# Kernel tuning notes

Hardware: AMD Instinct MI355X
Metric: run time of the kernel (lower is better)

Reference implementation:

```python
import jax, jax.numpy as jnp
import numpy as np

B, S, D = 4, 4096, 768
E, SLOTS = 16, 1  # n_experts, slots_per_expert
H = 4 * D


def setup_inputs() -> dict:
    key = jax.random.key(0)
    k = jax.random.split(key, 6)
    scale1 = 1.0 / np.sqrt(D)
    scale2 = 1.0 / np.sqrt(H)
    return {
        "x": jax.random.normal(k[0], (B, S, D), dtype=jnp.float32),
        "phi": jax.random.normal(k[1], (D, E * SLOTS), dtype=jnp.float32),
        "W1": jax.random.normal(k[2], (E, D, H), dtype=jnp.float32) * scale1,
        "b1": jnp.zeros((E, H), dtype=jnp.float32),
        "W2": jax.random.normal(k[3], (E, H, D), dtype=jnp.float32) * scale2,
        "b2": jnp.zeros((E, D), dtype=jnp.float32),
    }


def reference(x, phi, W1, b1, W2, b2):
    # logits: [B, S, E*SLOTS]
    logits = jnp.einsum("bsd,dn->bsn", x, phi)
    dispatch_weights = jax.nn.softmax(logits, axis=-1)  # over slots
    combine_weights = jax.nn.softmax(logits, axis=1)    # over sequence
    # xs: [B, E*SLOTS, D] = dispatch^T @ x
    xs = jnp.einsum("bsn,bsd->bnd", dispatch_weights, x)
    xs = xs.reshape(B, E, SLOTS, D)
    # per-expert FFN, batched over experts: GELU (exact, as torch nn.GELU default)
    h = jnp.einsum("bepd,edh->beph", xs, W1) + b1[None, :, None, :]
    h = jax.nn.gelu(h, approximate=False)
    ys = jnp.einsum("beph,ehd->bepd", h, W2) + b2[None, :, None, :]
    ys = ys.reshape(B, E * SLOTS, D)
    # combine: [B, S, D]
    y = jnp.einsum("bsn,bnd->bsd", combine_weights, ys)
    return y
```

## Files before the change

kernel.cpp:

```cpp
#include <hip/hip_runtime.h>
#include <math.h>

constexpr int B = 4, S = 4096, D = 768, E = 16, N = 16, H = 3072;
constexpr int HL = 96;
constexpr int NHC = H / HL;
constexpr int LBLK = 32;
constexpr int LPB = S / LBLK;

constexpr size_t OFF_LOG  = 0;
constexpr size_t OFF_PCM  = OFF_LOG + (size_t)B * S * N;
constexpr size_t OFF_PCS  = OFF_PCM + (size_t)B * LPB * N;
constexpr size_t OFF_CMAX = OFF_PCS + (size_t)B * LPB * N;
constexpr size_t OFF_CSUM = OFF_CMAX + (size_t)B * N;
constexpr size_t OFF_XSP  = OFF_CSUM + (size_t)B * N;
constexpr size_t OFF_XS   = OFF_XSP + (size_t)B * LPB * N * D;
constexpr size_t OFF_YSP  = OFF_XS + (size_t)B * N * D;
constexpr size_t OFF_YS   = OFF_YSP + (size_t)NHC * B * E * D;

__device__ __forceinline__ void fma4(float4& a, float s, const float4& w) {
    a.x = fmaf(s, w.x, a.x);
    a.y = fmaf(s, w.y, a.y);
    a.z = fmaf(s, w.z, a.z);
    a.w = fmaf(s, w.w, a.w);
}

__global__ __launch_bounds__(256) void k_lx(const float* __restrict__ x,
                                            const float* __restrict__ phi,
                                            float* __restrict__ logits,
                                            float* __restrict__ xsp,
                                            float* __restrict__ pcm,
                                            float* __restrict__ pcs) {
    __shared__ float ph[16][D];
    __shared__ float xr[LBLK][D + 4];
    __shared__ float dwl[LBLK][16];
    __shared__ float rm[16][16], rs[16][16];
    const int t = threadIdx.x;
    const int blk = blockIdx.x;
    const int b = blk / LPB;
    const int s0 = (blk % LPB) * LBLK;

#pragma unroll
    for (int i = 0; i < 12; ++i) {
        const int idx = i * 1024 + t * 4;
        const float4 v = *reinterpret_cast<const float4*>(phi + idx);
        const int d0 = idx >> 4;
        const int n0 = idx & 15;
        ph[n0 + 0][d0] = v.x;
        ph[n0 + 1][d0] = v.y;
        ph[n0 + 2][d0] = v.z;
        ph[n0 + 3][d0] = v.w;
    }
    const float* xsrc = x + ((size_t)b * S + s0) * D;
#pragma unroll
    for (int i = 0; i < 24; ++i) {
        const int idx = i * 256 + t;
        const int r = idx / 192, c = idx % 192;
        *reinterpret_cast<float4*>(&xr[r][c * 4]) =
            *reinterpret_cast<const float4*>(xsrc + (size_t)idx * 4);
    }
    __syncthreads();

    const int gid = t >> 4;
    const int ln = t & 15;
    const int r0 = gid * 2, r1 = r0 + 1;

    float4 a0[12], a1[12];
#pragma unroll
    for (int j = 0; j < 12; ++j) {
        a0[j] = *reinterpret_cast<const float4*>(&xr[r0][j * 64 + ln * 4]);
        a1[j] = *reinterpret_cast<const float4*>(&xr[r1][j * 64 + ln * 4]);
    }
    float p0[16], p1[16];
#pragma unroll
    for (int n = 0; n < 16; ++n) {
        float q0 = 0.f, q1 = 0.f;
#pragma unroll
        for (int j = 0; j < 12; ++j) {
            const float4 pv = *reinterpret_cast<const float4*>(&ph[n][j * 64 + ln * 4]);
            q0 = fmaf(a0[j].x, pv.x, q0); q1 = fmaf(a1[j].x, pv.x, q1);
            q0 = fmaf(a0[j].y, pv.y, q0); q1 = fmaf(a1[j].y, pv.y, q1);
            q0 = fmaf(a0[j].z, pv.z, q0); q1 = fmaf(a1[j].z, pv.z, q1);
            q0 = fmaf(a0[j].w, pv.w, q0); q1 = fmaf(a1[j].w, pv.w, q1);
        }
        p0[n] = q0; p1[n] = q1;
    }
#pragma unroll
    for (int m = 1; m < 16; m <<= 1) {
#pragma unroll
        for (int n = 0; n < 16; ++n) {
            p0[n] += __shfl_xor(p0[n], m, 64);
            p1[n] += __shfl_xor(p1[n], m, 64);
        }
    }
    float m0 = -1e30f, m1 = -1e30f;
#pragma unroll
    for (int n = 0; n < 16; ++n) { m0 = fmaxf(m0, p0[n]); m1 = fmaxf(m1, p1[n]); }
    float su0 = 0.f, su1 = 0.f;
#pragma unroll
    for (int n = 0; n < 16; ++n) { su0 += __expf(p0[n] - m0); su1 += __expf(p1[n] - m1); }
    const size_t o0 = ((size_t)b * S + s0 + r0) * N + ln;
    logits[o0] = p0[ln];
    logits[o0 + N] = p1[ln];
    dwl[r0][ln] = __expf(p0[ln] - m0) / su0;
    dwl[r1][ln] = __expf(p1[ln] - m1) / su1;

    const float mm = fmaxf(p0[ln], p1[ln]);
    rm[gid][ln] = mm;
    rs[gid][ln] = __expf(p0[ln] - mm) + __expf(p1[ln] - mm);
    __syncthreads();

    if (t < 16) {
        float M = -1e30f;
#pragma unroll
        for (int g = 0; g < 16; ++g) M = fmaxf(M, rm[g][t]);
        float SS = 0.f;
#pragma unroll
        for (int g = 0; g < 16; ++g) SS += rs[g][t] * __expf(rm[g][t] - M);
        pcm[blk * 16 + t] = M;
        pcs[blk * 16 + t] = SS;
    }

    if (t < 192) {
        const int d4 = t * 4;
        float4 a[16];
#pragma unroll
        for (int n = 0; n < 16; ++n) a[n] = float4{0.f, 0.f, 0.f, 0.f};
#pragma unroll 4
        for (int s = 0; s < LBLK; ++s) {
            const float4 xv = *reinterpret_cast<const float4*>(&xr[s][d4]);
#pragma unroll
            for (int n = 0; n < 16; ++n) {
                const float w = dwl[s][n];
                a[n].x = fmaf(w, xv.x, a[n].x);
                a[n].y = fmaf(w, xv.y, a[n].y);
                a[n].z = fmaf(w, xv.z, a[n].z);
                a[n].w = fmaf(w, xv.w, a[n].w);
            }
        }
        float* o = xsp + (size_t)blk * N * D + d4;
#pragma unroll
        for (int n = 0; n < 16; ++n)
            *reinterpret_cast<float4*>(o + (size_t)n * D) = a[n];
    }
}

__global__ __launch_bounds__(256) void k_xsred_cmerge(const float* __restrict__ xsp,
                                                      float* __restrict__ xs,
                                                      const float* __restrict__ pcm,
                                                      const float* __restrict__ pcs,
                                                      float* __restrict__ cmax,
                                                      float* __restrict__ csum) {
    const int t = threadIdx.x;
    if (blockIdx.x < 192) {
        const int i = blockIdx.x * 256 + t;
        const int b = i / (N * D);
        const int rem = i % (N * D);
        const float* p = xsp + (size_t)b * LPB * N * D + rem;
        float sum = 0.f;
#pragma unroll 4
        for (int c = 0; c < LPB; ++c) sum += p[(size_t)c * N * D];
        xs[i] = sum;
    } else if (t < 64) {
        const int b = t >> 4, n = t & 15;
        float M = -1e30f;
#pragma unroll 8
        for (int c = 0; c < LPB; ++c) M = fmaxf(M, pcm[((size_t)b * LPB + c) * 16 + n]);
        float SS = 0.f;
#pragma unroll 8
        for (int c = 0; c < LPB; ++c)
            SS += pcs[((size_t)b * LPB + c) * 16 + n] * __expf(pcm[((size_t)b * LPB + c) * 16 + n] - M);
        cmax[b * 16 + n] = M;
        csum[b * 16 + n] = SS;
    }
}

__global__ __launch_bounds__(384) void k_ffn(const float* __restrict__ xs,
                                             const float* __restrict__ W1,
                                             const float* __restrict__ b1,
                                             const float* __restrict__ W2,
                                             float* __restrict__ ysp) {
    __shared__ __align__(16) float xs_lds[D][4];
    __shared__ __align__(16) float red[32][HL][4];
    __shared__ __align__(16) float h_lds[HL][4];

    const int t = threadIdx.x;
    const int e = blockIdx.x / NHC;
    const int hc = blockIdx.x % NHC;
    const int h0 = hc * HL;

    for (int idx = t; idx < D; idx += 384) {
#pragma unroll
        for (int b = 0; b < 4; ++b)
            xs_lds[idx][b] = xs[((size_t)b * N + e) * D + idx];
    }
    __syncthreads();

    {
        const int q = t / 12;
        const int cg = t % 12;
        const int c4a = cg * 4, c4b = 48 + cg * 4;
        float4 aA[4], aB[4];
#pragma unroll
        for (int b = 0; b < 4; ++b) { aA[b] = float4{0,0,0,0}; aB[b] = float4{0,0,0,0}; }
        const float* w1p = W1 + ((size_t)e * D + (size_t)q * 24) * H + h0;
#pragma unroll 8
        for (int dd = 0; dd < 24; ++dd) {
            const float* row = w1p + (size_t)dd * H;
            const float4 wa = *reinterpret_cast<const float4*>(row + c4a);
            const float4 wb = *reinterpret_cast<const float4*>(row + c4b);
            const float* xv = &xs_lds[q * 24 + dd][0];
            const float x0 = xv[0], x1 = xv[1], x2 = xv[2], x3 = xv[3];
            fma4(aA[0], x0, wa); fma4(aB[0], x0, wb);
            fma4(aA[1], x1, wa); fma4(aB[1], x1, wb);
            fma4(aA[2], x2, wa); fma4(aB[2], x2, wb);
            fma4(aA[3], x3, wa); fma4(aB[3], x3, wb);
        }
        *reinterpret_cast<float4*>(&red[q][c4a + 0][0]) = float4{aA[0].x, aA[1].x, aA[2].x, aA[3].x};
        *reinterpret_cast<float4*>(&red[q][c4a + 1][0]) = float4{aA[0].y, aA[1].y, aA[2].y, aA[3].y};
        *reinterpret_cast<float4*>(&red[q][c4a + 2][0]) = float4{aA[0].z, aA[1].z, aA[2].z, aA[3].z};
        *reinterpret_cast<float4*>(&red[q][c4a + 3][0]) = float4{aA[0].w, aA[1].w, aA[2].w, aA[3].w};
        *reinterpret_cast<float4*>(&red[q][c4b + 0][0]) = float4{aB[0].x, aB[1].x, aB[2].x, aB[3].x};
        *reinterpret_cast<float4*>(&red[q][c4b + 1][0]) = float4{aB[0].y, aB[1].y, aB[2].y, aB[3].y};
        *reinterpret_cast<float4*>(&red[q][c4b + 2][0]) = float4{aB[0].z, aB[1].z, aB[2].z, aB[3].z};
        *reinterpret_cast<float4*>(&red[q][c4b + 3][0]) = float4{aB[0].w, aB[1].w, aB[2].w, aB[3].w};
    }
    __syncthreads();

    {
        const int col = t >> 2, b = t & 3;
        float s = 0.f;
#pragma unroll
        for (int q = 0; q < 32; ++q) s += red[q][col][b];
        s += b1[(size_t)e * H + h0 + col];
        s = 0.5f * s * (1.0f + erff(s * 0.70710678118654752f));
        h_lds[col][b] = s;
    }
    __syncthreads();

    const int kq = t / 96;
    const int dg = t % 96;
    const int d4a = dg * 4, d4b = 384 + dg * 4;
    float4 yA[4], yB[4];
#pragma unroll
    for (int b = 0; b < 4; ++b) { yA[b] = float4{0,0,0,0}; yB[b] = float4{0,0,0,0}; }
    {
        const float* w2p = W2 + ((size_t)e * H + h0 + (size_t)kq * 24) * D;
#pragma unroll 8
        for (int kk = 0; kk < 24; ++kk) {
            const float* row = w2p + (size_t)kk * D;
            const float4 wa = *reinterpret_cast<const float4*>(row + d4a);
            const float4 wb = *reinterpret_cast<const float4*>(row + d4b);
            const float* hv = &h_lds[kq * 24 + kk][0];
            fma4(yA[0], hv[0], wa); fma4(yB[0], hv[0], wb);
            fma4(yA[1], hv[1], wa); fma4(yB[1], hv[1], wb);
            fma4(yA[2], hv[2], wa); fma4(yB[2], hv[2], wb);
            fma4(yA[3], hv[3], wa); fma4(yB[3], hv[3], wb);
        }
    }
    float4* pb = reinterpret_cast<float4*>(&red[0][0][0]);
    __syncthreads();
    if (kq > 0) {
        const int base = ((kq - 1) * 96 + dg) * 8;
#pragma unroll
        for (int b = 0; b < 4; ++b) {
            pb[base + b * 2 + 0] = yA[b];
            pb[base + b * 2 + 1] = yB[b];
        }
    }
    __syncthreads();
    if (kq == 0) {
#pragma unroll
        for (int b = 0; b < 4; ++b) {
            float4 rA = yA[b], rB = yB[b];
#pragma unroll
            for (int p = 0; p < 3; ++p) {
                const int base = (p * 96 + dg) * 8 + b * 2;
                const float4 uA = pb[base + 0], uB = pb[base + 1];
                rA.x += uA.x; rA.y += uA.y; rA.z += uA.z; rA.w += uA.w;
                rB.x += uB.x; rB.y += uB.y; rB.z += uB.z; rB.w += uB.w;
            }
            float* o = ysp + (((size_t)hc * B + b) * E + e) * D;
            *reinterpret_cast<float4*>(o + d4a) = rA;
            *reinterpret_cast<float4*>(o + d4b) = rB;
        }
    }
}

__global__ __launch_bounds__(256) void k_ysred(const float* __restrict__ ysp,
                                               const float* __restrict__ b2,
                                               float* __restrict__ ys) {
    const int i4 = blockIdx.x * 256 + threadIdx.x;
    const int rem4 = i4 % (E * D / 4);
    float4 v = *reinterpret_cast<const float4*>(b2 + (size_t)rem4 * 4);
#pragma unroll 8
    for (int p = 0; p < NHC; ++p) {
        const float4 u = *reinterpret_cast<const float4*>(ysp + (size_t)p * B * E * D + (size_t)i4 * 4);
        v.x += u.x; v.y += u.y; v.z += u.z; v.w += u.w;
    }
    *reinterpret_cast<float4*>(ys + (size_t)i4 * 4) = v;
}

__global__ __launch_bounds__(192) void k_combine(const float* __restrict__ logits,
                                                 const float* __restrict__ cmax,
                                                 const float* __restrict__ csum,
                                                 const float* __restrict__ ys,
                                                 float* __restrict__ y) {
    const int blk = blockIdx.x;
    const int b = blk / (S / 8);
    const int s0 = (blk % (S / 8)) * 8;
    const int t = threadIdx.x;
    const int d4 = t * 4;

    float4 ysr[16];
    float cm[16], ci[16];
#pragma unroll
    for (int n = 0; n < 16; ++n) {
        ysr[n] = *reinterpret_cast<const float4*>(ys + ((size_t)b * N + n) * D + d4);
        cm[n] = cmax[b * N + n];
        ci[n] = 1.0f / csum[b * N + n];
    }
#pragma unroll
    for (int r = 0; r < 8; ++r) {
        const int s = s0 + r;
        const float* lrow = logits + ((size_t)b * S + s) * N;
        float4 acc{0, 0, 0, 0};
#pragma unroll
        for (int n = 0; n < 16; ++n) {
            const float cw = __expf(lrow[n] - cm[n]) * ci[n];
            acc.x = fmaf(cw, ysr[n].x, acc.x);
            acc.y = fmaf(cw, ysr[n].y, acc.y);
            acc.z = fmaf(cw, ysr[n].z, acc.z);
            acc.w = fmaf(cw, ysr[n].w, acc.w);
        }
        *reinterpret_cast<float4*>(y + ((size_t)b * S + s) * D + d4) = acc;
    }
}

extern "C" void kernel_launch(void* const* d_in, const int* in_sizes, int n_in,
                              void* d_out, int out_size, void* d_ws, size_t ws_size,
                              hipStream_t stream) {
    const float* x   = (const float*)d_in[0];
    const float* phi = (const float*)d_in[1];
    const float* W1  = (const float*)d_in[2];
    const float* b1  = (const float*)d_in[3];
    const float* W2  = (const float*)d_in[4];
    const float* b2  = (const float*)d_in[5];
    float* y = (float*)d_out;
    float* ws = (float*)d_ws;

    float* logits = ws + OFF_LOG;
    float* pcm    = ws + OFF_PCM;
    float* pcs    = ws + OFF_PCS;
    float* cmax   = ws + OFF_CMAX;
    float* csum   = ws + OFF_CSUM;
    float* xsp    = ws + OFF_XSP;
    float* xs     = ws + OFF_XS;
    float* ysp    = ws + OFF_YSP;
    float* ys     = ws + OFF_YS;

    k_lx<<<B * LPB, 256, 0, stream>>>(x, phi, logits, xsp, pcm, pcs);
    k_xsred_cmerge<<<193, 256, 0, stream>>>(xsp, xs, pcm, pcs, cmax, csum);
    k_ffn<<<E * NHC, 384, 0, stream>>>(xs, W1, b1, W2, ysp);
    k_ysred<<<48, 256, 0, stream>>>(ysp, b2, ys);
    k_combine<<<B * (S / 8), 192, 0, stream>>>(logits, cmax, csum, ys, y);
}
```

Baseline: 154.1 us.

## Double-buffer nontemporal weight loads in expert FFN with deeper per-thread K chunks

```diff
diff --git a/kernel.cpp b/kernel.cpp
--- a/kernel.cpp
+++ b/kernel.cpp
@@ -17,7 +17,12 @@
 constexpr size_t OFF_YSP  = OFF_XS + (size_t)B * N * D;
 constexpr size_t OFF_YS   = OFF_YSP + (size_t)NHC * B * E * D;
 
-__device__ __forceinline__ void fma4(float4& a, float s, const float4& w) {
+typedef float vf4 __attribute__((ext_vector_type(4)));
+
+__device__ __forceinline__ vf4 ntl(const float* p) {
+    return __builtin_nontemporal_load(reinterpret_cast<const vf4*>(p));
+}
+__device__ __forceinline__ void fma4(float4& a, float s, const vf4& w) {
     a.x = fmaf(s, w.x, a.x);
     a.y = fmaf(s, w.y, a.y);
     a.z = fmaf(s, w.z, a.z);
@@ -180,7 +185,7 @@
                                              const float* __restrict__ W2,
                                              float* __restrict__ ysp) {
     __shared__ __align__(16) float xs_lds[D][4];
-    __shared__ __align__(16) float red[32][HL][4];
+    __shared__ __align__(16) float red_lds[16][HL][4];
     __shared__ __align__(16) float h_lds[HL][4];
 
     const int t = threadIdx.x;
@@ -196,33 +201,42 @@
     __syncthreads();
 
     {
-        const int q = t / 12;
-        const int cg = t % 12;
-        const int c4a = cg * 4, c4b = 48 + cg * 4;
-        float4 aA[4], aB[4];
-#pragma unroll
-        for (int b = 0; b < 4; ++b) { aA[b] = float4{0,0,0,0}; aB[b] = float4{0,0,0,0}; }
-        const float* w1p = W1 + ((size_t)e * D + (size_t)q * 24) * H + h0;
-#pragma unroll 8
-        for (int dd = 0; dd < 24; ++dd) {
-            const float* row = w1p + (size_t)dd * H;
-            const float4 wa = *reinterpret_cast<const float4*>(row + c4a);
-            const float4 wb = *reinterpret_cast<const float4*>(row + c4b);
-            const float* xv = &xs_lds[q * 24 + dd][0];
-            const float x0 = xv[0], x1 = xv[1], x2 = xv[2], x3 = xv[3];
-            fma4(aA[0], x0, wa); fma4(aB[0], x0, wb);
-            fma4(aA[1], x1, wa); fma4(aB[1], x1, wb);
-            fma4(aA[2], x2, wa); fma4(aB[2], x2, wb);
-            fma4(aA[3], x3, wa); fma4(aB[3], x3, wb);
-        }
-        *reinterpret_cast<float4*>(&red[q][c4a + 0][0]) = float4{aA[0].x, aA[1].x, aA[2].x, aA[3].x};
-        *reinterpret_cast<float4*>(&red[q][c4a + 1][0]) = float4{aA[0].y, aA[1].y, aA[2].y, aA[3].y};
-        *reinterpret_cast<float4*>(&red[q][c4a + 2][0]) = float4{aA[0].z, aA[1].z, aA[2].z, aA[3].z};
-        *reinterpret_cast<float4*>(&red[q][c4a + 3][0]) = float4{aA[0].w, aA[1].w, aA[2].w, aA[3].w};
-        *reinterpret_cast<float4*>(&red[q][c4b + 0][0]) = float4{aB[0].x, aB[1].x, aB[2].x, aB[3].x};
-        *reinterpret_cast<float4*>(&red[q][c4b + 1][0]) = float4{aB[0].y, aB[1].y, aB[2].y, aB[3].y};
-        *reinterpret_cast<float4*>(&red[q][c4b + 2][0]) = float4{aB[0].z, aB[1].z, aB[2].z, aB[3].z};
-        *reinterpret_cast<float4*>(&red[q][c4b + 3][0]) = float4{aB[0].w, aB[1].w, aB[2].w, aB[3].w};
+        const int c4 = (t % 24) * 4;
+        const int q = t / 24;
+        const float* w1p = W1 + ((size_t)e * D + (size_t)q * 48) * H + h0 + c4;
+        float4 a0{0,0,0,0}, a1{0,0,0,0}, a2{0,0,0,0}, a3{0,0,0,0};
+        vf4 bufA[8], bufB[8];
+#pragma unroll
+        for (int i = 0; i < 8; ++i) bufA[i] = ntl(w1p + (size_t)i * H);
+
+#define P1_STAGE(CUR, NXT, CH, PRE)                                          \
+        {                                                                    \
+            if (PRE) {                                                       \
+                _Pragma("unroll")                                            \
+                for (int i = 0; i < 8; ++i)                                  \
+                    NXT[i] = ntl(w1p + (size_t)((CH + 1) * 8 + i) * H);      \
+            }                                                                \
+            _Pragma("unroll")                                                \
+            for (int i = 0; i < 8; ++i) {                                    \
+                const float* xv = &xs_lds[q * 48 + CH * 8 + i][0];           \
+                fma4(a0, xv[0], CUR[i]);                                     \
+                fma4(a1, xv[1], CUR[i]);                                     \
+                fma4(a2, xv[2], CUR[i]);                                     \
+                fma4(a3, xv[3], CUR[i]);                                     \
+            }                                                                \
+        }
+        P1_STAGE(bufA, bufB, 0, 1)
+        P1_STAGE(bufB, bufA, 1, 1)
+        P1_STAGE(bufA, bufB, 2, 1)
+        P1_STAGE(bufB, bufA, 3, 1)
+        P1_STAGE(bufA, bufB, 4, 1)
+        P1_STAGE(bufB, bufA, 5, 0)
+#undef P1_STAGE
+
+        *reinterpret_cast<float4*>(&red_lds[q][c4 + 0][0]) = float4{a0.x, a1.x, a2.x, a3.x};
+        *reinterpret_cast<float4*>(&red_lds[q][c4 + 1][0]) = float4{a0.y, a1.y, a2.y, a3.y};
+        *reinterpret_cast<float4*>(&red_lds[q][c4 + 2][0]) = float4{a0.z, a1.z, a2.z, a3.z};
+        *reinterpret_cast<float4*>(&red_lds[q][c4 + 3][0]) = float4{a0.w, a1.w, a2.w, a3.w};
     }
     __syncthreads();
 
@@ -230,59 +244,73 @@
         const int col = t >> 2, b = t & 3;
         float s = 0.f;
 #pragma unroll
-        for (int q = 0; q < 32; ++q) s += red[q][col][b];
+        for (int q = 0; q < 16; ++q) s += red_lds[q][col][b];
         s += b1[(size_t)e * H + h0 + col];
         s = 0.5f * s * (1.0f + erff(s * 0.70710678118654752f));
         h_lds[col][b] = s;
     }
     __syncthreads();
 
-    const int kq = t / 96;
-    const int dg = t % 96;
-    const int d4a = dg * 4, d4b = 384 + dg * 4;
-    float4 yA[4], yB[4];
-#pragma unroll
-    for (int b = 0; b < 4; ++b) { yA[b] = float4{0,0,0,0}; yB[b] = float4{0,0,0,0}; }
+    const int dgrp = t % 192;
+    const int kq = t / 192;
+    float4 y0{0,0,0,0}, y1{0,0,0,0}, y2{0,0,0,0}, y3{0,0,0,0};
     {
-        const float* w2p = W2 + ((size_t)e * H + h0 + (size_t)kq * 24) * D;
-#pragma unroll 8
-        for (int kk = 0; kk < 24; ++kk) {
-            const float* row = w2p + (size_t)kk * D;
-            const float4 wa = *reinterpret_cast<const float4*>(row + d4a);
-            const float4 wb = *reinterpret_cast<const float4*>(row + d4b);
-            const float* hv = &h_lds[kq * 24 + kk][0];
-            fma4(yA[0], hv[0], wa); fma4(yB[0], hv[0], wb);
-            fma4(yA[1], hv[1], wa); fma4(yB[1], hv[1], wb);
-            fma4(yA[2], hv[2], wa); fma4(yB[2], hv[2], wb);
-            fma4(yA[3], hv[3], wa); fma4(yB[3], hv[3], wb);
-        }
-    }
-    float4* pb = reinterpret_cast<float4*>(&red[0][0][0]);
-    __syncthreads();
-    if (kq > 0) {
-        const int base = ((kq - 1) * 96 + dg) * 8;
-#pragma unroll
-        for (int b = 0; b < 4; ++b) {
-            pb[base + b * 2 + 0] = yA[b];
-            pb[base + b * 2 + 1] = yB[b];
-        }
+        const float* w2p = W2 + ((size_t)e * H + h0 + (size_t)kq * 48) * D + dgrp * 4;
+        vf4 bufA[8], bufB[8];
+#pragma unroll
+        for (int i = 0; i < 8; ++i) bufA[i] = ntl(w2p + (size_t)i * D);
+
+#define P2_STAGE(CUR, NXT, CH, PRE)                                          \
+        {                                                                    \
+            if (PRE) {                                                       \
+                _Pragma("unroll")                                            \
+                for (int i = 0; i < 8; ++i)                                  \
+                    NXT[i] = ntl(w2p + (size_t)((CH + 1) * 8 + i) * D);      \
+            }                                                                \
+            _Pragma("unroll")                                                \
+            for (int i = 0; i < 8; ++i) {                                    \
+                const float* hv = &h_lds[kq * 48 + CH * 8 + i][0];           \
+                fma4(y0, hv[0], CUR[i]);                                     \
+                fma4(y1, hv[1], CUR[i]);                                     \
+                fma4(y2, hv[2], CUR[i]);                                     \
+                fma4(y3, hv[3], CUR[i]);                                     \
+            }                                                                \
+        }
+        P2_STAGE(bufA, bufB, 0, 1)
+        P2_STAGE(bufB, bufA, 1, 1)
+        P2_STAGE(bufA, bufB, 2, 1)
+        P2_STAGE(bufB, bufA, 3, 1)
+        P2_STAGE(bufA, bufB, 4, 1)
+        P2_STAGE(bufB, bufA, 5, 0)
+#undef P2_STAGE
+    }
+
+    float4* pbuf = reinterpret_cast<float4*>(&xs_lds[0][0]);
+    __syncthreads();
+    if (kq == 1) {
+        pbuf[dgrp * 4 + 0] = y0;
+        pbuf[dgrp * 4 + 1] = y1;
+        pbuf[dgrp * 4 + 2] = y2;
+        pbuf[dgrp * 4 + 3] = y3;
     }
     __syncthreads();
     if (kq == 0) {
-#pragma unroll
-        for (int b = 0; b < 4; ++b) {
-            float4 rA = yA[b], rB = yB[b];
-#pragma unroll
-            for (int p = 0; p < 3; ++p) {
-                const int base = (p * 96 + dg) * 8 + b * 2;
-                const float4 uA = pb[base + 0], uB = pb[base + 1];
-                rA.x += uA.x; rA.y += uA.y; rA.z += uA.z; rA.w += uA.w;
-                rB.x += uB.x; rB.y += uB.y; rB.z += uB.z; rB.w += uB.w;
-            }
-            float* o = ysp + (((size_t)hc * B + b) * E + e) * D;
-            *reinterpret_cast<float4*>(o + d4a) = rA;
-            *reinterpret_cast<float4*>(o + d4b) = rB;
-        }
+        float4 r0 = pbuf[dgrp * 4 + 0];
+        float4 r1 = pbuf[dgrp * 4 + 1];
+        float4 r2 = pbuf[dgrp * 4 + 2];
+        float4 r3 = pbuf[dgrp * 4 + 3];
+        r0.x += y0.x; r0.y += y0.y; r0.z += y0.z; r0.w += y0.w;
+        r1.x += y1.x; r1.y += y1.y; r1.z += y1.z; r1.w += y1.w;
+        r2.x += y2.x; r2.y += y2.y; r2.z += y2.z; r2.w += y2.w;
+        r3.x += y3.x; r3.y += y3.y; r3.z += y3.z; r3.w += y3.w;
+        float* o0 = ysp + (((size_t)hc * B + 0) * E + e) * D + dgrp * 4;
+        float* o1 = ysp + (((size_t)hc * B + 1) * E + e) * D + dgrp * 4;
+        float* o2 = ysp + (((size_t)hc * B + 2) * E + e) * D + dgrp * 4;
+        float* o3 = ysp + (((size_t)hc * B + 3) * E + e) * D + dgrp * 4;
+        *reinterpret_cast<float4*>(o0) = r0;
+        *reinterpret_cast<float4*>(o1) = r1;
+        *reinterpret_cast<float4*>(o2) = r2;
+        *reinterpret_cast<float4*>(o3) = r3;
     }
 }
 
```

New measurement: 140.2 us. 1.1x faster.
